# Kernel optimization log

Hardware: AMD Instinct MI355X
Metric: run time of the kernel (lower is better)

The kernel has to match this reference:

```python
import jax, jax.numpy as jnp
import numpy as np

MARGIN = 0.3
EPS = 1e-6  # torch.nn.functional.pairwise_distance eps


def setup_inputs() -> dict:
    key = jax.random.key(0)
    k1, k2 = jax.random.split(key)
    B, D, C = 8192, 256, 512
    embeddings = jax.random.normal(k1, (B, D), dtype=jnp.float32)
    labels = jax.random.randint(k2, (B,), 0, C, dtype=jnp.int64)
    return {"embeddings": embeddings, "labels": labels}


def reference(embeddings, labels):
    B = embeddings.shape[0]
    # pairwise squared L2 via GEMM
    dot = embeddings @ embeddings.T                      # [B, B]
    sq = jnp.diag(dot)[:, None] + jnp.diag(dot)[None, :] - 2.0 * dot
    dist_sq = jnp.clip(sq, 0.0)

    same = labels[:, None] == labels[None, :]            # [B, B] bool
    eye = jnp.eye(B, dtype=bool)
    pos_mask = same & ~eye
    neg_mask = ~same

    valid = pos_mask.any(axis=1) & neg_mask.any(axis=1)  # [B]
    INF = dist_sq.max() + 1.0

    hardest_pos_idx = jnp.argmax(dist_sq * pos_mask.astype(dist_sq.dtype), axis=1)
    hardest_neg_idx = jnp.argmin(dist_sq + same.astype(dist_sq.dtype) * INF, axis=1)

    a = embeddings
    p = embeddings[hardest_pos_idx]
    n = embeddings[hardest_neg_idx]
    # torch pairwise_distance: ||x1 - x2 + eps||_2
    d_ap = jnp.linalg.norm(a - p + EPS, axis=1)
    d_an = jnp.linalg.norm(a - n + EPS, axis=1)
    per_anchor = jnp.maximum(d_ap - d_an + MARGIN, 0.0)

    v = valid.astype(per_anchor.dtype)
    n_valid = v.sum()
    loss = jnp.where(n_valid > 0, (per_anchor * v).sum() / jnp.maximum(n_valid, 1.0), 0.0)
    return loss
```

## Files before the change

kernel.cpp:

```cpp
#include <hip/hip_runtime.h>
#include <math.h>

#define NB 8192
#define ND 256
#define MARGIN_F 0.3f
#define EPS_F 1e-6f
#define BIAS_F 512.0f
#define NFIN 2048

typedef __attribute__((ext_vector_type(8))) short bf16x8;
typedef __attribute__((ext_vector_type(4))) float f32x4;

__device__ __forceinline__ unsigned short f2bf(float x) {
    unsigned int u = __float_as_uint(x);
    return (unsigned short)((u + 0x7fffu + ((u >> 16) & 1u)) >> 16);
}

__device__ __forceinline__ void gld16(const void* g, void* l) {
    __builtin_amdgcn_global_load_lds(
        (const __attribute__((address_space(1))) void*)g,
        (__attribute__((address_space(3))) void*)l, 16, 0, 0);
}

__global__ __launch_bounds__(512) void prep_k(const float* __restrict__ emb,
                                              unsigned short* __restrict__ ehi,
                                              float* __restrict__ sqnb,
                                              unsigned int* __restrict__ pos_key,
                                              unsigned int* __restrict__ neg_key) {
    __shared__ float sm[8][16];
    const int tid = threadIdx.x;
    const int tk = tid >> 6;
    const int lane = tid & 63;
    const int q = lane >> 4;
    const int lx = lane & 15;
    const int row = blockIdx.x * 16 + lx;
    const int k = tk * 32 + q * 8;

    const float4 v0 = *reinterpret_cast<const float4*>(&emb[(size_t)row * ND + k]);
    const float4 v1 = *reinterpret_cast<const float4*>(&emb[(size_t)row * ND + k + 4]);
    ushort4 h0, h1;
    h0.x = f2bf(v0.x); h0.y = f2bf(v0.y); h0.z = f2bf(v0.z); h0.w = f2bf(v0.w);
    h1.x = f2bf(v1.x); h1.y = f2bf(v1.y); h1.z = f2bf(v1.z); h1.w = f2bf(v1.w);
    *reinterpret_cast<ushort4*>(&ehi[(size_t)blockIdx.x * 4096 + tid * 8])     = h0;
    *reinterpret_cast<ushort4*>(&ehi[(size_t)blockIdx.x * 4096 + tid * 8 + 4]) = h1;

    if (tid >= 32 && tid < 48) pos_key[blockIdx.x * 16 + (tid - 32)] = 0u;
    if (tid >= 48 && tid < 64) neg_key[blockIdx.x * 16 + (tid - 48)] = 0xFFFFFFFFu;

    float s = v0.x * v0.x + v0.y * v0.y + v0.z * v0.z + v0.w * v0.w
            + v1.x * v1.x + v1.y * v1.y + v1.z * v1.z + v1.w * v1.w;
    s += __shfl_xor(s, 16, 64);
    s += __shfl_xor(s, 32, 64);
    if (q == 0) sm[tk][lx] = s;
    __syncthreads();
    if (tid < 16) {
        float t = 0.0f;
#pragma unroll
        for (int wv = 0; wv < 8; ++wv) t += sm[wv][tid];
        sqnb[blockIdx.x * 16 + tid] = t + BIAS_F;
    }
}

template <bool DIAG>
__device__ __forceinline__ void mine_tile(
        const f32x4 (&acc)[2][4], const float (&sqjc)[4], const int (&lblc)[4],
        const unsigned (&enc)[4], const int* __restrict__ lbl_i_s,
        unsigned (&pmax)[8], unsigned (&nmin)[8],
        int i_base, int jb, int wrow, int q, int lx) {
#pragma unroll
    for (int tr = 0; tr < 2; ++tr) {
#pragma unroll
        for (int reg = 0; reg < 4; ++reg) {
            const int r = tr * 4 + reg;
            const int rowb = wrow + tr * 16 + q * 4 + reg;
            const int lab = lbl_i_s[rowb];
            unsigned pk[4], nk[4];
#pragma unroll
            for (int tc = 0; tc < 4; ++tc) {
                const float v = fmaf(-2.0f, acc[tr][tc][reg], sqjc[tc]);
                const unsigned key = (__float_as_uint(v) & 0xFFFFE000u) | enc[tc];
                const bool same = (lblc[tc] == lab);
                bool pc = same;
                if (DIAG) pc = same && ((jb + tc * 16 + lx) != (i_base + rowb));
                pk[tc] = pc ? key : 0u;
                nk[tc] = same ? 0xFFFFFFFFu : key;
            }
            const unsigned pa = pk[0] >= pk[1] ? pk[0] : pk[1];
            const unsigned pb = pk[2] >= pk[3] ? pk[2] : pk[3];
            const unsigned pm = pa >= pb ? pa : pb;
            pmax[r] = pmax[r] >= pm ? pmax[r] : pm;
            const unsigned na = nk[0] <= nk[1] ? nk[0] : nk[1];
            const unsigned nb = nk[2] <= nk[3] ? nk[2] : nk[3];
            const unsigned nm = na <= nb ? na : nb;
            nmin[r] = nmin[r] <= nm ? nmin[r] : nm;
        }
    }
}

__global__ __launch_bounds__(256, 4) void pair_k(
        const unsigned short* __restrict__ ehi, const float* __restrict__ sqnb,
        const int* __restrict__ labels,
        unsigned int* __restrict__ pos_key, unsigned int* __restrict__ neg_key) {
    __shared__ short Bsh[32 * 512];
    __shared__ int   lbl_i_s[128];

    const int tid = threadIdx.x;
    const int w = tid >> 6;
    const int lane = tid & 63;
    const int q = lane >> 4;
    const int lx = lane & 15;
    const int bid = blockIdx.x;
    const int slice = bid & 15;
    const int i_base = (bid >> 4) * 128;
    const int wrow = w * 32;
    const int g0 = (i_base >> 4) + w * 2;

    if (tid < 128) lbl_i_s[tid] = labels[i_base + tid];

    unsigned pmax[8], nmin[8];
#pragma unroll
    for (int r = 0; r < 8; ++r) { pmax[r] = 0u; nmin[r] = 0xFFFFFFFFu; }

#pragma unroll 1
    for (int jt = 0; jt < 8; ++jt) {
        const int jb = slice * 512 + jt * 64;
        __syncthreads();
        {
            const unsigned short* srcB = ehi + (size_t)(jb >> 4) * 4096;
#pragma unroll
            for (int p = 0; p < 8; ++p)
                gld16(srcB + ((size_t)p * 256 + tid) * 8, Bsh + (p * 256 + tid) * 8);
        }
        int lblc[4]; float sqjc[4]; unsigned enc[4];
#pragma unroll
        for (int tc = 0; tc < 4; ++tc) {
            const int jj = jb + tc * 16 + lx;
            lblc[tc] = labels[jj];
            sqjc[tc] = sqnb[jj];
            enc[tc] = 8191u - (unsigned)jj;
        }
        bf16x8 a0[2], a1[2];
#pragma unroll
        for (int tr = 0; tr < 2; ++tr)
            a0[tr] = *(const bf16x8*)&ehi[((size_t)(g0 + tr) * 8 + 0) * 512 + lane * 8];
        __syncthreads();

        f32x4 acc[2][4];
#pragma unroll
        for (int a = 0; a < 2; ++a)
#pragma unroll
            for (int b = 0; b < 4; ++b) acc[a][b] = (f32x4){0.f, 0.f, 0.f, 0.f};

#pragma unroll 1
        for (int kb2 = 0; kb2 < 4; ++kb2) {
            const int kbe = kb2 * 2, kbo = kbe + 1;
#pragma unroll
            for (int tr = 0; tr < 2; ++tr)
                a1[tr] = *(const bf16x8*)&ehi[((size_t)(g0 + tr) * 8 + kbo) * 512 + lane * 8];
            {
                bf16x8 bh[4];
#pragma unroll
                for (int tc = 0; tc < 4; ++tc)
                    bh[tc] = *(const bf16x8*)&Bsh[(tc * 8 + kbe) * 512 + lane * 8];
#pragma unroll
                for (int tr = 0; tr < 2; ++tr)
#pragma unroll
                    for (int tc = 0; tc < 4; ++tc)
                        acc[tr][tc] = __builtin_amdgcn_mfma_f32_16x16x32_bf16(
                            a0[tr], bh[tc], acc[tr][tc], 0, 0, 0);
            }
            const int kbn = (kbe + 2) & 7;
#pragma unroll
            for (int tr = 0; tr < 2; ++tr)
                a0[tr] = *(const bf16x8*)&ehi[((size_t)(g0 + tr) * 8 + kbn) * 512 + lane * 8];
            {
                bf16x8 bh[4];
#pragma unroll
                for (int tc = 0; tc < 4; ++tc)
                    bh[tc] = *(const bf16x8*)&Bsh[(tc * 8 + kbo) * 512 + lane * 8];
#pragma unroll
                for (int tr = 0; tr < 2; ++tr)
#pragma unroll
                    for (int tc = 0; tc < 4; ++tc)
                        acc[tr][tc] = __builtin_amdgcn_mfma_f32_16x16x32_bf16(
                            a1[tr], bh[tc], acc[tr][tc], 0, 0, 0);
            }
        }

        if ((unsigned)(jb - i_base) < 128u)
            mine_tile<true>(acc, sqjc, lblc, enc, lbl_i_s, pmax, nmin, i_base, jb, wrow, q, lx);
        else
            mine_tile<false>(acc, sqjc, lblc, enc, lbl_i_s, pmax, nmin, i_base, jb, wrow, q, lx);
    }

#pragma unroll
    for (int r = 0; r < 8; ++r) {
        unsigned pm = pmax[r], nm = nmin[r];
#pragma unroll
        for (int mm = 1; mm < 16; mm <<= 1) {
            const unsigned pm2 = __shfl_xor(pm, mm, 64);
            const unsigned nm2 = __shfl_xor(nm, mm, 64);
            pm = pm >= pm2 ? pm : pm2;
            nm = nm <= nm2 ? nm : nm2;
        }
        if (lx == r) {
            const int row = i_base + wrow + (r >> 2) * 16 + q * 4 + (r & 3);
            atomicMax(&pos_key[row], pm);
            atomicMin(&neg_key[row], nm);
        }
    }
}

__global__ __launch_bounds__(256) void final_k(
        const float* __restrict__ emb,
        const unsigned int* __restrict__ pos_key, const unsigned int* __restrict__ neg_key,
        float* __restrict__ pbsum, float* __restrict__ pbcnt) {
    __shared__ float ssum[4], scnt[4];
    const int w = threadIdx.x >> 6;
    const int lane = threadIdx.x & 63;
    const int i = blockIdx.x * 4 + w;

    const unsigned pk = pos_key[i], nk = neg_key[i];
    const int pi = 8191 - (int)(pk & 8191u);
    const int ni = 8191 - (int)(nk & 8191u);
    const bool valid = (pk != 0u) && (nk != 0xFFFFFFFFu);

    const float4 av  = *reinterpret_cast<const float4*>(&emb[(size_t)i  * ND + lane * 4]);
    const float4 pvv = *reinterpret_cast<const float4*>(&emb[(size_t)pi * ND + lane * 4]);
    const float4 nvv = *reinterpret_cast<const float4*>(&emb[(size_t)ni * ND + lane * 4]);
    float sap, san;
    {
        const float d0 = av.x - pvv.x + EPS_F, d1 = av.y - pvv.y + EPS_F;
        const float d2 = av.z - pvv.z + EPS_F, d3 = av.w - pvv.w + EPS_F;
        sap = d0 * d0 + d1 * d1 + d2 * d2 + d3 * d3;
        const float e0 = av.x - nvv.x + EPS_F, e1 = av.y - nvv.y + EPS_F;
        const float e2 = av.z - nvv.z + EPS_F, e3 = av.w - nvv.w + EPS_F;
        san = e0 * e0 + e1 * e1 + e2 * e2 + e3 * e3;
    }
#pragma unroll
    for (int m = 32; m; m >>= 1) {
        sap += __shfl_down(sap, m, 64);
        san += __shfl_down(san, m, 64);
    }
    if (lane == 0) {
        const float per = fmaxf(sqrtf(sap) - sqrtf(san) + MARGIN_F, 0.0f);
        ssum[w] = valid ? per : 0.0f;
        scnt[w] = valid ? 1.0f : 0.0f;
    }
    __syncthreads();
    if (threadIdx.x == 0) {
        pbsum[blockIdx.x] = ssum[0] + ssum[1] + ssum[2] + ssum[3];
        pbcnt[blockIdx.x] = scnt[0] + scnt[1] + scnt[2] + scnt[3];
    }
}

__global__ __launch_bounds__(256) void reduce_k(const float* __restrict__ pbsum,
                                                const float* __restrict__ pbcnt,
                                                float* __restrict__ out) {
    __shared__ float fs[4], fc[4];
    const int tid = threadIdx.x;
    float s = 0.0f, c = 0.0f;
#pragma unroll
    for (int r = 0; r < NFIN / 256; ++r) {
        s += pbsum[r * 256 + tid];
        c += pbcnt[r * 256 + tid];
    }
#pragma unroll
    for (int m = 32; m; m >>= 1) { s += __shfl_down(s, m, 64); c += __shfl_down(c, m, 64); }
    const int wv = tid >> 6, lane = tid & 63;
    if (lane == 0) { fs[wv] = s; fc[wv] = c; }
    __syncthreads();
    if (tid == 0) {
        const float S = fs[0] + fs[1] + fs[2] + fs[3];
        const float C = fc[0] + fc[1] + fc[2] + fc[3];
        out[0] = (C > 0.0f) ? (S / fmaxf(C, 1.0f)) : 0.0f;
    }
}

extern "C" void kernel_launch(void* const* d_in, const int* in_sizes, int n_in,
                              void* d_out, int out_size, void* d_ws, size_t ws_size,
                              hipStream_t stream) {
    const float* emb = (const float*)d_in[0];
    const int* labels = (const int*)d_in[1];
    float* out = (float*)d_out;

    char* ws = (char*)d_ws;
    unsigned short* ehi = (unsigned short*)ws;
    float* sqnb = (float*)(ws + (size_t)NB * ND * 2);
    unsigned int* pos_key = (unsigned int*)(sqnb + NB);
    unsigned int* neg_key = pos_key + NB;
    float* pbsum = (float*)(neg_key + NB);
    float* pbcnt = pbsum + NFIN;

    hipLaunchKernelGGL(prep_k, dim3(NB / 16), dim3(512), 0, stream,
                       emb, ehi, sqnb, pos_key, neg_key);
    hipLaunchKernelGGL(pair_k, dim3(1024), dim3(256), 0, stream,
                       ehi, sqnb, labels, pos_key, neg_key);
    hipLaunchKernelGGL(final_k, dim3(NFIN), dim3(256), 0, stream,
                       emb, pos_key, neg_key, pbsum, pbcnt);
    hipLaunchKernelGGL(reduce_k, dim3(1), dim3(256), 0, stream, pbsum, pbcnt, out);
}
```

Baseline: 114.3 us.

## Hold A tile in registers, widen column tile, double-buffer B in LDS

The pair kernel now loads the whole 32x256 A fragment into registers once, with -2 scaling folded in by flipping the bf16 sign bit (and adjusting the exponent). B tiles widen to 128 columns and are double-buffered in LDS by K halves, so loads overlap MFMA work. Accumulators start at the column norm, which removes the FMA in mining, and row labels are cached in registers. Occupancy drops from 4 to 2 blocks per CU to make room for the extra registers, and the bit trick assumes no bf16 exponent edge cases.

Result: no change. 114.3 us (+0.0%).

```diff
diff --git a/kernel.cpp b/kernel.cpp
--- a/kernel.cpp
+++ b/kernel.cpp
@@ -10,6 +10,7 @@
 
 typedef __attribute__((ext_vector_type(8))) short bf16x8;
 typedef __attribute__((ext_vector_type(4))) float f32x4;
+typedef __attribute__((ext_vector_type(4))) unsigned int u32x4;
 
 __device__ __forceinline__ unsigned short f2bf(float x) {
     unsigned int u = __float_as_uint(x);
@@ -63,8 +64,8 @@
 
 template <bool DIAG>
 __device__ __forceinline__ void mine_tile(
-        const f32x4 (&acc)[2][4], const float (&sqjc)[4], const int (&lblc)[4],
-        const unsigned (&enc)[4], const int* __restrict__ lbl_i_s,
+        const f32x4 (&acc)[2][8], const int (&lblc)[8], const unsigned (&enc)[8],
+        const int (&labr)[8],
         unsigned (&pmax)[8], unsigned (&nmin)[8],
         int i_base, int jb, int wrow, int q, int lx) {
 #pragma unroll
@@ -72,37 +73,45 @@
 #pragma unroll
         for (int reg = 0; reg < 4; ++reg) {
             const int r = tr * 4 + reg;
-            const int rowb = wrow + tr * 16 + q * 4 + reg;
-            const int lab = lbl_i_s[rowb];
-            unsigned pk[4], nk[4];
-#pragma unroll
-            for (int tc = 0; tc < 4; ++tc) {
-                const float v = fmaf(-2.0f, acc[tr][tc][reg], sqjc[tc]);
+            const int lab = labr[r];
+            const int rowg = i_base + wrow + tr * 16 + q * 4 + reg;
+            unsigned pk[8], nk[8];
+#pragma unroll
+            for (int tc = 0; tc < 8; ++tc) {
+                const float v = acc[tr][tc][reg];
                 const unsigned key = (__float_as_uint(v) & 0xFFFFE000u) | enc[tc];
                 const bool same = (lblc[tc] == lab);
                 bool pc = same;
-                if (DIAG) pc = same && ((jb + tc * 16 + lx) != (i_base + rowb));
+                if (DIAG) pc = same && ((jb + tc * 16 + lx) != rowg);
                 pk[tc] = pc ? key : 0u;
                 nk[tc] = same ? 0xFFFFFFFFu : key;
             }
             const unsigned pa = pk[0] >= pk[1] ? pk[0] : pk[1];
             const unsigned pb = pk[2] >= pk[3] ? pk[2] : pk[3];
-            const unsigned pm = pa >= pb ? pa : pb;
+            const unsigned pc2 = pk[4] >= pk[5] ? pk[4] : pk[5];
+            const unsigned pd = pk[6] >= pk[7] ? pk[6] : pk[7];
+            const unsigned pe = pa >= pb ? pa : pb;
+            const unsigned pf = pc2 >= pd ? pc2 : pd;
+            const unsigned pm = pe >= pf ? pe : pf;
             pmax[r] = pmax[r] >= pm ? pmax[r] : pm;
             const unsigned na = nk[0] <= nk[1] ? nk[0] : nk[1];
             const unsigned nb = nk[2] <= nk[3] ? nk[2] : nk[3];
-            const unsigned nm = na <= nb ? na : nb;
+            const unsigned nc = nk[4] <= nk[5] ? nk[4] : nk[5];
+            const unsigned nd = nk[6] <= nk[7] ? nk[6] : nk[7];
+            const unsigned ne = na <= nb ? na : nb;
+            const unsigned nf = nc <= nd ? nc : nd;
+            const unsigned nm = ne <= nf ? ne : nf;
             nmin[r] = nmin[r] <= nm ? nmin[r] : nm;
         }
     }
 }
 
-__global__ __launch_bounds__(256, 4) void pair_k(
+__global__ __launch_bounds__(256, 2) void pair_k(
         const unsigned short* __restrict__ ehi, const float* __restrict__ sqnb,
         const int* __restrict__ labels,
         unsigned int* __restrict__ pos_key, unsigned int* __restrict__ neg_key) {
-    __shared__ short Bsh[32 * 512];
-    __shared__ int   lbl_i_s[128];
+    __shared__ short Bsh[2][16384];
+    __shared__ __align__(16) int lbl_i_s[128];
 
     const int tid = threadIdx.x;
     const int w = tid >> 6;
@@ -113,84 +122,107 @@
     const int slice = bid & 15;
     const int i_base = (bid >> 4) * 128;
     const int wrow = w * 32;
-    const int g0 = (i_base >> 4) + w * 2;
+    const int ga0 = (i_base >> 4) + w * 2;
 
     if (tid < 128) lbl_i_s[tid] = labels[i_base + tid];
 
+    {
+        const unsigned short* src = ehi + (size_t)(slice * 32) * 4096;
+#pragma unroll
+        for (int p = 0; p < 8; ++p)
+            gld16(src + (size_t)p * 4096 + tid * 8, &Bsh[0][(p * 256 + tid) * 8]);
+    }
+
+    bf16x8 a[2][8];
+#pragma unroll
+    for (int tr = 0; tr < 2; ++tr)
+#pragma unroll
+        for (int s = 0; s < 8; ++s) {
+            union { u32x4 u; bf16x8 h; } cv;
+            cv.u = *reinterpret_cast<const u32x4*>(
+                &ehi[((size_t)(ga0 + tr) * 8 + s) * 512 + lane * 8]);
+            cv.u = (cv.u ^ 0x80008000u) + 0x00800080u;
+            a[tr][s] = cv.h;
+        }
+
     unsigned pmax[8], nmin[8];
 #pragma unroll
     for (int r = 0; r < 8; ++r) { pmax[r] = 0u; nmin[r] = 0xFFFFFFFFu; }
 
+    __syncthreads();
+
+    int labr[8];
+    {
+        const int4 l0 = *reinterpret_cast<const int4*>(&lbl_i_s[wrow + q * 4]);
+        const int4 l1 = *reinterpret_cast<const int4*>(&lbl_i_s[wrow + 16 + q * 4]);
+        labr[0] = l0.x; labr[1] = l0.y; labr[2] = l0.z; labr[3] = l0.w;
+        labr[4] = l1.x; labr[5] = l1.y; labr[6] = l1.z; labr[7] = l1.w;
+    }
+
 #pragma unroll 1
-    for (int jt = 0; jt < 8; ++jt) {
-        const int jb = slice * 512 + jt * 64;
-        __syncthreads();
-        {
-            const unsigned short* srcB = ehi + (size_t)(jb >> 4) * 4096;
-#pragma unroll
-            for (int p = 0; p < 8; ++p)
-                gld16(srcB + ((size_t)p * 256 + tid) * 8, Bsh + (p * 256 + tid) * 8);
-        }
-        int lblc[4]; float sqjc[4]; unsigned enc[4];
-#pragma unroll
-        for (int tc = 0; tc < 4; ++tc) {
+    for (int jt = 0; jt < 4; ++jt) {
+        const int jb = slice * 512 + jt * 128;
+
+        int lblc[8]; unsigned enc[8];
+        f32x4 acc[2][8];
+#pragma unroll
+        for (int tc = 0; tc < 8; ++tc) {
             const int jj = jb + tc * 16 + lx;
             lblc[tc] = labels[jj];
-            sqjc[tc] = sqnb[jj];
             enc[tc] = 8191u - (unsigned)jj;
-        }
-        bf16x8 a0[2], a1[2];
-#pragma unroll
-        for (int tr = 0; tr < 2; ++tr)
-            a0[tr] = *(const bf16x8*)&ehi[((size_t)(g0 + tr) * 8 + 0) * 512 + lane * 8];
+            const float sj = sqnb[jj];
+            acc[0][tc] = (f32x4){sj, sj, sj, sj};
+            acc[1][tc] = (f32x4){sj, sj, sj, sj};
+        }
+
+        {
+            const unsigned short* src = ehi + (size_t)(jb >> 4) * 4096 + 2048;
+#pragma unroll
+            for (int p = 0; p < 8; ++p)
+                gld16(src + (size_t)p * 4096 + tid * 8, &Bsh[1][(p * 256 + tid) * 8]);
+        }
+        __builtin_amdgcn_s_setprio(1);
+#pragma unroll
+        for (int kb = 0; kb < 4; ++kb) {
+#pragma unroll
+            for (int tc = 0; tc < 8; ++tc) {
+                const bf16x8 bh = *reinterpret_cast<const bf16x8*>(
+                    &Bsh[0][(tc * 4 + kb) * 512 + lane * 8]);
+                acc[0][tc] = __builtin_amdgcn_mfma_f32_16x16x32_bf16(
+                    a[0][kb], bh, acc[0][tc], 0, 0, 0);
+                acc[1][tc] = __builtin_amdgcn_mfma_f32_16x16x32_bf16(
+                    a[1][kb], bh, acc[1][tc], 0, 0, 0);
+            }
+        }
+        __builtin_amdgcn_s_setprio(0);
         __syncthreads();
 
-        f32x4 acc[2][4];
-#pragma unroll
-        for (int a = 0; a < 2; ++a)
-#pragma unroll
-            for (int b = 0; b < 4; ++b) acc[a][b] = (f32x4){0.f, 0.f, 0.f, 0.f};
-
-#pragma unroll 1
-        for (int kb2 = 0; kb2 < 4; ++kb2) {
-            const int kbe = kb2 * 2, kbo = kbe + 1;
-#pragma unroll
-            for (int tr = 0; tr < 2; ++tr)
-                a1[tr] = *(const bf16x8*)&ehi[((size_t)(g0 + tr) * 8 + kbo) * 512 + lane * 8];
-            {
-                bf16x8 bh[4];
-#pragma unroll
-                for (int tc = 0; tc < 4; ++tc)
-                    bh[tc] = *(const bf16x8*)&Bsh[(tc * 8 + kbe) * 512 + lane * 8];
-#pragma unroll
-                for (int tr = 0; tr < 2; ++tr)
-#pragma unroll
-                    for (int tc = 0; tc < 4; ++tc)
-                        acc[tr][tc] = __builtin_amdgcn_mfma_f32_16x16x32_bf16(
-                            a0[tr], bh[tc], acc[tr][tc], 0, 0, 0);
+        if (jt < 3) {
+            const unsigned short* src = ehi + (size_t)((jb + 128) >> 4) * 4096;
+#pragma unroll
+            for (int p = 0; p < 8; ++p)
+                gld16(src + (size_t)p * 4096 + tid * 8, &Bsh[0][(p * 256 + tid) * 8]);
+        }
+        __builtin_amdgcn_s_setprio(1);
+#pragma unroll
+        for (int kb = 0; kb < 4; ++kb) {
+#pragma unroll
+            for (int tc = 0; tc < 8; ++tc) {
+                const bf16x8 bh = *reinterpret_cast<const bf16x8*>(
+                    &Bsh[1][(tc * 4 + kb) * 512 + lane * 8]);
+                acc[0][tc] = __builtin_amdgcn_mfma_f32_16x16x32_bf16(
+                    a[0][4 + kb], bh, acc[0][tc], 0, 0, 0);
+                acc[1][tc] = __builtin_amdgcn_mfma_f32_16x16x32_bf16(
+                    a[1][4 + kb], bh, acc[1][tc], 0, 0, 0);
             }
-            const int kbn = (kbe + 2) & 7;
-#pragma unroll
-            for (int tr = 0; tr < 2; ++tr)
-                a0[tr] = *(const bf16x8*)&ehi[((size_t)(g0 + tr) * 8 + kbn) * 512 + lane * 8];
-            {
-                bf16x8 bh[4];
-#pragma unroll
-                for (int tc = 0; tc < 4; ++tc)
-                    bh[tc] = *(const bf16x8*)&Bsh[(tc * 8 + kbo) * 512 + lane * 8];
-#pragma unroll
-                for (int tr = 0; tr < 2; ++tr)
-#pragma unroll
-                    for (int tc = 0; tc < 4; ++tc)
-                        acc[tr][tc] = __builtin_amdgcn_mfma_f32_16x16x32_bf16(
-                            a1[tr], bh[tc], acc[tr][tc], 0, 0, 0);
-            }
-        }
-
-        if ((unsigned)(jb - i_base) < 128u)
-            mine_tile<true>(acc, sqjc, lblc, enc, lbl_i_s, pmax, nmin, i_base, jb, wrow, q, lx);
+        }
+        __builtin_amdgcn_s_setprio(0);
+        __syncthreads();
+
+        if (jb == i_base)
+            mine_tile<true>(acc, lblc, enc, labr, pmax, nmin, i_base, jb, wrow, q, lx);
         else
-            mine_tile<false>(acc, sqjc, lblc, enc, lbl_i_s, pmax, nmin, i_base, jb, wrow, q, lx);
+            mine_tile<false>(acc, lblc, enc, labr, pmax, nmin, i_base, jb, wrow, q, lx);
     }
 
 #pragma unroll
```

## Enlarge pair tiles, keep A in registers, double-buffer B, fold sq-norm into accumulator

Applied to the files above, without the earlier changes.

The pair kernel now gives each block 256 rows, and each wave 64 rows held entirely in registers with the sign flipped so the MFMA computes -dot. The B tiles are double-buffered in LDS in K halves, and the accumulator is initialised with the column squared norm, so mining reads the distance directly and compares floats with fmax/fmin. The separate reduce kernel is removed: final_k uses a last-block ticket to do the global reduction, saving one launch. The larger register footprint (64 bf16x8 A fragments plus 16 accumulators) may cut occupancy. The tiling also changes to 32 slices of 256 columns.

Result: slower. 251.7 us (+120.2%).

```diff
diff --git a/kernel.cpp b/kernel.cpp
--- a/kernel.cpp
+++ b/kernel.cpp
@@ -7,9 +7,11 @@
 #define EPS_F 1e-6f
 #define BIAS_F 512.0f
 #define NFIN 2048
+#define NEG_INIT 0x7F800000u
 
 typedef __attribute__((ext_vector_type(8))) short bf16x8;
 typedef __attribute__((ext_vector_type(4))) float f32x4;
+typedef __attribute__((ext_vector_type(4))) unsigned int u32x4;
 
 __device__ __forceinline__ unsigned short f2bf(float x) {
     unsigned int u = __float_as_uint(x);
@@ -26,7 +28,8 @@
                                               unsigned short* __restrict__ ehi,
                                               float* __restrict__ sqnb,
                                               unsigned int* __restrict__ pos_key,
-                                              unsigned int* __restrict__ neg_key) {
+                                              unsigned int* __restrict__ neg_key,
+                                              unsigned int* __restrict__ ticket) {
     __shared__ float sm[8][16];
     const int tid = threadIdx.x;
     const int tk = tid >> 6;
@@ -45,7 +48,8 @@
     *reinterpret_cast<ushort4*>(&ehi[(size_t)blockIdx.x * 4096 + tid * 8 + 4]) = h1;
 
     if (tid >= 32 && tid < 48) pos_key[blockIdx.x * 16 + (tid - 32)] = 0u;
-    if (tid >= 48 && tid < 64) neg_key[blockIdx.x * 16 + (tid - 48)] = 0xFFFFFFFFu;
+    if (tid >= 48 && tid < 64) neg_key[blockIdx.x * 16 + (tid - 48)] = NEG_INIT;
+    if (blockIdx.x == 0 && tid == 0) atomicExch(ticket, 0u);
 
     float s = v0.x * v0.x + v0.y * v0.y + v0.z * v0.z + v0.w * v0.w
             + v1.x * v1.x + v1.y * v1.y + v1.z * v1.z + v1.w * v1.w;
@@ -63,36 +67,32 @@
 
 template <bool DIAG>
 __device__ __forceinline__ void mine_tile(
-        const f32x4 (&acc)[2][4], const float (&sqjc)[4], const int (&lblc)[4],
-        const unsigned (&enc)[4], const int* __restrict__ lbl_i_s,
-        unsigned (&pmax)[8], unsigned (&nmin)[8],
-        int i_base, int jb, int wrow, int q, int lx) {
-#pragma unroll
-    for (int tr = 0; tr < 2; ++tr) {
+        const f32x4 (&acc)[4][4], const int (&lblc)[4], const unsigned (&enc)[4],
+        const int (&labr)[16], float (&pmax)[16], float (&nmin)[16],
+        int jb, int wr_base, int q, int lx) {
+    const float NEGF = __uint_as_float(NEG_INIT);
+#pragma unroll
+    for (int tr = 0; tr < 4; ++tr) {
 #pragma unroll
         for (int reg = 0; reg < 4; ++reg) {
             const int r = tr * 4 + reg;
-            const int rowb = wrow + tr * 16 + q * 4 + reg;
-            const int lab = lbl_i_s[rowb];
-            unsigned pk[4], nk[4];
+            const int lab = labr[r];
+            const int rowg = wr_base + tr * 16 + q * 4 + reg;
+            float pk[4], nk[4];
 #pragma unroll
             for (int tc = 0; tc < 4; ++tc) {
-                const float v = fmaf(-2.0f, acc[tr][tc][reg], sqjc[tc]);
-                const unsigned key = (__float_as_uint(v) & 0xFFFFE000u) | enc[tc];
+                const unsigned kb = (__float_as_uint(acc[tr][tc][reg]) & 0xFFFFE000u) | enc[tc];
+                const float keyf = __uint_as_float(kb);
                 const bool same = (lblc[tc] == lab);
                 bool pc = same;
-                if (DIAG) pc = same && ((jb + tc * 16 + lx) != (i_base + rowb));
-                pk[tc] = pc ? key : 0u;
-                nk[tc] = same ? 0xFFFFFFFFu : key;
+                if (DIAG) pc = same && ((jb + tc * 16 + lx) != rowg);
+                pk[tc] = pc ? keyf : 0.0f;
+                nk[tc] = same ? NEGF : keyf;
             }
-            const unsigned pa = pk[0] >= pk[1] ? pk[0] : pk[1];
-            const unsigned pb = pk[2] >= pk[3] ? pk[2] : pk[3];
-            const unsigned pm = pa >= pb ? pa : pb;
-            pmax[r] = pmax[r] >= pm ? pmax[r] : pm;
-            const unsigned na = nk[0] <= nk[1] ? nk[0] : nk[1];
-            const unsigned nb = nk[2] <= nk[3] ? nk[2] : nk[3];
-            const unsigned nm = na <= nb ? na : nb;
-            nmin[r] = nmin[r] <= nm ? nmin[r] : nm;
+            const float t0 = fmaxf(fmaxf(pk[0], pk[1]), pk[2]);
+            pmax[r] = fmaxf(fmaxf(t0, pk[3]), pmax[r]);
+            const float t1 = fminf(fminf(nk[0], nk[1]), nk[2]);
+            nmin[r] = fminf(fminf(t1, nk[3]), nmin[r]);
         }
     }
 }
@@ -101,8 +101,8 @@
         const unsigned short* __restrict__ ehi, const float* __restrict__ sqnb,
         const int* __restrict__ labels,
         unsigned int* __restrict__ pos_key, unsigned int* __restrict__ neg_key) {
-    __shared__ short Bsh[32 * 512];
-    __shared__ int   lbl_i_s[128];
+    __shared__ short Bsh[2][8192];
+    __shared__ __align__(16) int lbl_i_s[256];
 
     const int tid = threadIdx.x;
     const int w = tid >> 6;
@@ -110,103 +110,115 @@
     const int q = lane >> 4;
     const int lx = lane & 15;
     const int bid = blockIdx.x;
-    const int slice = bid & 15;
-    const int i_base = (bid >> 4) * 128;
-    const int wrow = w * 32;
-    const int g0 = (i_base >> 4) + w * 2;
-
-    if (tid < 128) lbl_i_s[tid] = labels[i_base + tid];
-
-    unsigned pmax[8], nmin[8];
-#pragma unroll
-    for (int r = 0; r < 8; ++r) { pmax[r] = 0u; nmin[r] = 0xFFFFFFFFu; }
+    const int slice = bid & 31;
+    const int i_base = (bid >> 5) * 256;
+    const int wrow = w * 64;
+    const int wr_base = i_base + wrow;
+    const int ga0 = wr_base >> 4;
+
+    lbl_i_s[tid] = labels[i_base + tid];
+
+#define STAGE(JT, KH, BUF)                                                      \
+    do {                                                                        \
+        const unsigned short* _src =                                            \
+            ehi + ((size_t)((slice * 16 + (JT) * 4) * 8 + (KH) * 4)) * 512;     \
+        _Pragma("unroll")                                                       \
+        for (int p = 0; p < 4; ++p)                                             \
+            gld16(_src + ((size_t)(p * 8 + w)) * 512 + lane * 8,                \
+                  &Bsh[BUF][(p * 4 + w) * 512 + lane * 8]);                     \
+    } while (0)
+
+    STAGE(0, 0, 0);
+
+    bf16x8 a[4][8];
+#pragma unroll
+    for (int tr = 0; tr < 4; ++tr)
+#pragma unroll
+        for (int s = 0; s < 8; ++s) {
+            union { u32x4 u; bf16x8 h; } cv;
+            cv.u = *reinterpret_cast<const u32x4*>(
+                &ehi[((size_t)(ga0 + tr) * 8 + s) * 512 + lane * 8]);
+            cv.u = (cv.u ^ 0x80008000u) + 0x00800080u;
+            a[tr][s] = cv.h;
+        }
+
+    float pmax[16], nmin[16];
+    const float NEGF = __uint_as_float(NEG_INIT);
+#pragma unroll
+    for (int r = 0; r < 16; ++r) { pmax[r] = 0.0f; nmin[r] = NEGF; }
+
+    __syncthreads();
+
+    int labr[16];
+#pragma unroll
+    for (int tr = 0; tr < 4; ++tr) {
+        const int4 l = *reinterpret_cast<const int4*>(&lbl_i_s[wrow + tr * 16 + q * 4]);
+        labr[tr * 4 + 0] = l.x; labr[tr * 4 + 1] = l.y;
+        labr[tr * 4 + 2] = l.z; labr[tr * 4 + 3] = l.w;
+    }
+
+#define PHASE(BUF, S0)                                                          \
+    do {                                                                        \
+        __builtin_amdgcn_s_setprio(1);                                          \
+        _Pragma("unroll")                                                       \
+        for (int kb = 0; kb < 4; ++kb) {                                        \
+            _Pragma("unroll")                                                   \
+            for (int tc = 0; tc < 4; ++tc) {                                    \
+                const bf16x8 bh = *reinterpret_cast<const bf16x8*>(             \
+                    &Bsh[BUF][(tc * 4 + kb) * 512 + lane * 8]);                 \
+                _Pragma("unroll")                                               \
+                for (int tr = 0; tr < 4; ++tr)                                  \
+                    acc[tr][tc] = __builtin_amdgcn_mfma_f32_16x16x32_bf16(      \
+                        a[tr][(S0) + kb], bh, acc[tr][tc], 0, 0, 0);            \
+            }                                                                   \
+        }                                                                       \
+        __builtin_amdgcn_s_setprio(0);                                          \
+    } while (0)
 
 #pragma unroll 1
-    for (int jt = 0; jt < 8; ++jt) {
-        const int jb = slice * 512 + jt * 64;
-        __syncthreads();
-        {
-            const unsigned short* srcB = ehi + (size_t)(jb >> 4) * 4096;
-#pragma unroll
-            for (int p = 0; p < 8; ++p)
-                gld16(srcB + ((size_t)p * 256 + tid) * 8, Bsh + (p * 256 + tid) * 8);
-        }
-        int lblc[4]; float sqjc[4]; unsigned enc[4];
+    for (int jt = 0; jt < 4; ++jt) {
+        const int jb = slice * 256 + jt * 64;
+
+        STAGE(jt, 1, 1);
+
+        int lblc[4]; unsigned enc[4];
+        f32x4 acc[4][4];
 #pragma unroll
         for (int tc = 0; tc < 4; ++tc) {
             const int jj = jb + tc * 16 + lx;
             lblc[tc] = labels[jj];
-            sqjc[tc] = sqnb[jj];
             enc[tc] = 8191u - (unsigned)jj;
-        }
-        bf16x8 a0[2], a1[2];
-#pragma unroll
-        for (int tr = 0; tr < 2; ++tr)
-            a0[tr] = *(const bf16x8*)&ehi[((size_t)(g0 + tr) * 8 + 0) * 512 + lane * 8];
+            const float sj = sqnb[jj];
+#pragma unroll
+            for (int tr = 0; tr < 4; ++tr) acc[tr][tc] = (f32x4){sj, sj, sj, sj};
+        }
+
+        PHASE(0, 0);
         __syncthreads();
-
-        f32x4 acc[2][4];
-#pragma unroll
-        for (int a = 0; a < 2; ++a)
-#pragma unroll
-            for (int b = 0; b < 4; ++b) acc[a][b] = (f32x4){0.f, 0.f, 0.f, 0.f};
-
-#pragma unroll 1
-        for (int kb2 = 0; kb2 < 4; ++kb2) {
-            const int kbe = kb2 * 2, kbo = kbe + 1;
-#pragma unroll
-            for (int tr = 0; tr < 2; ++tr)
-                a1[tr] = *(const bf16x8*)&ehi[((size_t)(g0 + tr) * 8 + kbo) * 512 + lane * 8];
-            {
-                bf16x8 bh[4];
-#pragma unroll
-                for (int tc = 0; tc < 4; ++tc)
-                    bh[tc] = *(const bf16x8*)&Bsh[(tc * 8 + kbe) * 512 + lane * 8];
-#pragma unroll
-                for (int tr = 0; tr < 2; ++tr)
-#pragma unroll
-                    for (int tc = 0; tc < 4; ++tc)
-                        acc[tr][tc] = __builtin_amdgcn_mfma_f32_16x16x32_bf16(
-                            a0[tr], bh[tc], acc[tr][tc], 0, 0, 0);
-            }
-            const int kbn = (kbe + 2) & 7;
-#pragma unroll
-            for (int tr = 0; tr < 2; ++tr)
-                a0[tr] = *(const bf16x8*)&ehi[((size_t)(g0 + tr) * 8 + kbn) * 512 + lane * 8];
-            {
-                bf16x8 bh[4];
-#pragma unroll
-                for (int tc = 0; tc < 4; ++tc)
-                    bh[tc] = *(const bf16x8*)&Bsh[(tc * 8 + kbo) * 512 + lane * 8];
-#pragma unroll
-                for (int tr = 0; tr < 2; ++tr)
-#pragma unroll
-                    for (int tc = 0; tc < 4; ++tc)
-                        acc[tr][tc] = __builtin_amdgcn_mfma_f32_16x16x32_bf16(
-                            a1[tr], bh[tc], acc[tr][tc], 0, 0, 0);
-            }
-        }
-
-        if ((unsigned)(jb - i_base) < 128u)
-            mine_tile<true>(acc, sqjc, lblc, enc, lbl_i_s, pmax, nmin, i_base, jb, wrow, q, lx);
+        if (jt < 3) STAGE(jt + 1, 0, 0);
+        PHASE(1, 4);
+        __syncthreads();
+
+        if (jb == wr_base)
+            mine_tile<true>(acc, lblc, enc, labr, pmax, nmin, jb, wr_base, q, lx);
         else
-            mine_tile<false>(acc, sqjc, lblc, enc, lbl_i_s, pmax, nmin, i_base, jb, wrow, q, lx);
-    }
-
-#pragma unroll
-    for (int r = 0; r < 8; ++r) {
-        unsigned pm = pmax[r], nm = nmin[r];
+            mine_tile<false>(acc, lblc, enc, labr, pmax, nmin, jb, wr_base, q, lx);
+    }
+#undef STAGE
+#undef PHASE
+
+#pragma unroll
+    for (int r = 0; r < 16; ++r) {
+        float pm = pmax[r], nm = nmin[r];
 #pragma unroll
         for (int mm = 1; mm < 16; mm <<= 1) {
-            const unsigned pm2 = __shfl_xor(pm, mm, 64);
-            const unsigned nm2 = __shfl_xor(nm, mm, 64);
-            pm = pm >= pm2 ? pm : pm2;
-            nm = nm <= nm2 ? nm : nm2;
+            pm = fmaxf(pm, __shfl_xor(pm, mm, 64));
+            nm = fminf(nm, __shfl_xor(nm, mm, 64));
         }
         if (lx == r) {
-            const int row = i_base + wrow + (r >> 2) * 16 + q * 4 + (r & 3);
-            atomicMax(&pos_key[row], pm);
-            atomicMin(&neg_key[row], nm);
+            const int row = wr_base + (r >> 2) * 16 + q * 4 + (r & 3);
+            atomicMax(&pos_key[row], __float_as_uint(pm));
+            atomicMin(&neg_key[row], __float_as_uint(nm));
         }
     }
 }
@@ -214,16 +226,19 @@
 __global__ __launch_bounds__(256) void final_k(
         const float* __restrict__ emb,
         const unsigned int* __restrict__ pos_key, const unsigned int* __restrict__ neg_key,
-        float* __restrict__ pbsum, float* __restrict__ pbcnt) {
+        float* __restrict__ pbsum, float* __restrict__ pbcnt,
+        unsigned int* __restrict__ ticket, float* __restrict__ out) {
     __shared__ float ssum[4], scnt[4];
-    const int w = threadIdx.x >> 6;
-    const int lane = threadIdx.x & 63;
+    __shared__ unsigned int last;
+    const int tid = threadIdx.x;
+    const int w = tid >> 6;
+    const int lane = tid & 63;
     const int i = blockIdx.x * 4 + w;
 
     const unsigned pk = pos_key[i], nk = neg_key[i];
     const int pi = 8191 - (int)(pk & 8191u);
     const int ni = 8191 - (int)(nk & 8191u);
-    const bool valid = (pk != 0u) && (nk != 0xFFFFFFFFu);
+    const bool valid = (pk != 0u) && (nk != NEG_INIT);
 
     const float4 av  = *reinterpret_cast<const float4*>(&emb[(size_t)i  * ND + lane * 4]);
     const float4 pvv = *reinterpret_cast<const float4*>(&emb[(size_t)pi * ND + lane * 4]);
@@ -248,32 +263,30 @@
         scnt[w] = valid ? 1.0f : 0.0f;
     }
     __syncthreads();
-    if (threadIdx.x == 0) {
+    if (tid == 0) {
         pbsum[blockIdx.x] = ssum[0] + ssum[1] + ssum[2] + ssum[3];
         pbcnt[blockIdx.x] = scnt[0] + scnt[1] + scnt[2] + scnt[3];
-    }
-}
-
-__global__ __launch_bounds__(256) void reduce_k(const float* __restrict__ pbsum,
-                                                const float* __restrict__ pbcnt,
-                                                float* __restrict__ out) {
-    __shared__ float fs[4], fc[4];
-    const int tid = threadIdx.x;
-    float s = 0.0f, c = 0.0f;
-#pragma unroll
-    for (int r = 0; r < NFIN / 256; ++r) {
-        s += pbsum[r * 256 + tid];
-        c += pbcnt[r * 256 + tid];
-    }
-#pragma unroll
-    for (int m = 32; m; m >>= 1) { s += __shfl_down(s, m, 64); c += __shfl_down(c, m, 64); }
-    const int wv = tid >> 6, lane = tid & 63;
-    if (lane == 0) { fs[wv] = s; fc[wv] = c; }
+        __threadfence();
+        last = (atomicAdd(ticket, 1u) == (unsigned)(NFIN - 1)) ? 1u : 0u;
+    }
     __syncthreads();
-    if (tid == 0) {
-        const float S = fs[0] + fs[1] + fs[2] + fs[3];
-        const float C = fc[0] + fc[1] + fc[2] + fc[3];
-        out[0] = (C > 0.0f) ? (S / fmaxf(C, 1.0f)) : 0.0f;
+    if (last != 0u) {
+        __shared__ float fs[4], fc[4];
+        float s = 0.0f, c = 0.0f;
+#pragma unroll
+        for (int r = 0; r < NFIN / 256; ++r) {
+            s += atomicAdd(&pbsum[r * 256 + tid], 0.0f);
+            c += atomicAdd(&pbcnt[r * 256 + tid], 0.0f);
+        }
+#pragma unroll
+        for (int m = 32; m; m >>= 1) { s += __shfl_down(s, m, 64); c += __shfl_down(c, m, 64); }
+        if (lane == 0) { fs[w] = s; fc[w] = c; }
+        __syncthreads();
+        if (tid == 0) {
+            const float S = fs[0] + fs[1] + fs[2] + fs[3];
+            const float C = fc[0] + fc[1] + fc[2] + fc[3];
+            out[0] = (C > 0.0f) ? (S / fmaxf(C, 1.0f)) : 0.0f;
+        }
     }
 }
 
@@ -291,12 +304,12 @@
     unsigned int* neg_key = pos_key + NB;
     float* pbsum = (float*)(neg_key + NB);
     float* pbcnt = pbsum + NFIN;
+    unsigned int* ticket = (unsigned int*)(pbcnt + NFIN);
 
     hipLaunchKernelGGL(prep_k, dim3(NB / 16), dim3(512), 0, stream,
-                       emb, ehi, sqnb, pos_key, neg_key);
+                       emb, ehi, sqnb, pos_key, neg_key, ticket);
     hipLaunchKernelGGL(pair_k, dim3(1024), dim3(256), 0, stream,
                        ehi, sqnb, labels, pos_key, neg_key);
     hipLaunchKernelGGL(final_k, dim3(NFIN), dim3(256), 0, stream,
-                       emb, pos_key, neg_key, pbsum, pbcnt);
-    hipLaunchKernelGGL(reduce_k, dim3(1), dim3(256), 0, stream, pbsum, pbcnt, out);
-}
+                       emb, pos_key, neg_key, pbsum, pbcnt, ticket, out);
+}
```

## Double-buffer B tiles by K-half and fold column norms into MFMA accumulator init

Applied to the files above, without the earlier changes.

The B tile in LDS is split into two K-halves held in separate buffers. The next half's global-to-LDS load is issued while MFMAs run on the current half, and all A fragments for a half are preloaded, with setprio raised around the MFMA blocks. The -2·dot+sq_j epilogue is removed by starting the accumulator at -0.5·sq_j. Mining then works on float min/max keys, and negative-biased floats are reinterpreted so the existing unsigned atomics still order correctly. This adds register pressure from the preloaded A fragments. Correctness depends on the bias keeping every accumulator value negative so that float and uint orderings stay consistent.

Measured after the change: 116.5 us. About the same (+1.9%).

```diff
diff --git a/kernel.cpp b/kernel.cpp
--- a/kernel.cpp
+++ b/kernel.cpp
@@ -63,10 +63,12 @@
 
 template <bool DIAG>
 __device__ __forceinline__ void mine_tile(
-        const f32x4 (&acc)[2][4], const float (&sqjc)[4], const int (&lblc)[4],
-        const unsigned (&enc)[4], const int* __restrict__ lbl_i_s,
-        unsigned (&pmax)[8], unsigned (&nmin)[8],
+        const f32x4 (&acc)[2][4], const int (&lblc)[4], const unsigned (&enc)[4],
+        const int* __restrict__ lbl_i_s,
+        float (&pkey)[8], float (&nkey)[8],
         int i_base, int jb, int wrow, int q, int lx) {
+    const float PINF = __uint_as_float(0x7F800000u);
+    const float NINF = __uint_as_float(0xFF800000u);
 #pragma unroll
     for (int tr = 0; tr < 2; ++tr) {
 #pragma unroll
@@ -74,25 +76,21 @@
             const int r = tr * 4 + reg;
             const int rowb = wrow + tr * 16 + q * 4 + reg;
             const int lab = lbl_i_s[rowb];
-            unsigned pk[4], nk[4];
+            float pk[4], nk[4];
 #pragma unroll
             for (int tc = 0; tc < 4; ++tc) {
-                const float v = fmaf(-2.0f, acc[tr][tc][reg], sqjc[tc]);
-                const unsigned key = (__float_as_uint(v) & 0xFFFFE000u) | enc[tc];
+                const float keyf = __uint_as_float(
+                    (__float_as_uint(acc[tr][tc][reg]) & 0xFFFFE000u) | enc[tc]);
                 const bool same = (lblc[tc] == lab);
                 bool pc = same;
                 if (DIAG) pc = same && ((jb + tc * 16 + lx) != (i_base + rowb));
-                pk[tc] = pc ? key : 0u;
-                nk[tc] = same ? 0xFFFFFFFFu : key;
+                pk[tc] = pc ? keyf : PINF;
+                nk[tc] = same ? NINF : keyf;
             }
-            const unsigned pa = pk[0] >= pk[1] ? pk[0] : pk[1];
-            const unsigned pb = pk[2] >= pk[3] ? pk[2] : pk[3];
-            const unsigned pm = pa >= pb ? pa : pb;
-            pmax[r] = pmax[r] >= pm ? pmax[r] : pm;
-            const unsigned na = nk[0] <= nk[1] ? nk[0] : nk[1];
-            const unsigned nb = nk[2] <= nk[3] ? nk[2] : nk[3];
-            const unsigned nm = na <= nb ? na : nb;
-            nmin[r] = nmin[r] <= nm ? nmin[r] : nm;
+            const float t0 = fminf(fminf(pk[0], pk[1]), pk[2]);
+            pkey[r] = fminf(fminf(t0, pk[3]), pkey[r]);
+            const float t1 = fmaxf(fmaxf(nk[0], nk[1]), nk[2]);
+            nkey[r] = fmaxf(fmaxf(t1, nk[3]), nkey[r]);
         }
     }
 }
@@ -101,8 +99,8 @@
         const unsigned short* __restrict__ ehi, const float* __restrict__ sqnb,
         const int* __restrict__ labels,
         unsigned int* __restrict__ pos_key, unsigned int* __restrict__ neg_key) {
-    __shared__ short Bsh[32 * 512];
-    __shared__ int   lbl_i_s[128];
+    __shared__ __align__(16) short Bsh[2][8192];
+    __shared__ int lbl_i_s[128];
 
     const int tid = threadIdx.x;
     const int w = tid >> 6;
@@ -117,21 +115,40 @@
 
     if (tid < 128) lbl_i_s[tid] = labels[i_base + tid];
 
-    unsigned pmax[8], nmin[8];
-#pragma unroll
-    for (int r = 0; r < 8; ++r) { pmax[r] = 0u; nmin[r] = 0xFFFFFFFFu; }
+#define STAGE(JT, KH, BUF)                                                            \
+    do {                                                                              \
+        _Pragma("unroll")                                                             \
+        for (int p = 0; p < 4; ++p)                                                   \
+            gld16(ehi + (size_t)((slice * 32 + (JT) * 4 + p) * 8 + (KH) * 4) * 512    \
+                      + tid * 8,                                                      \
+                  &Bsh[BUF][(p * 256 + tid) * 8]);                                    \
+    } while (0)
+
+#define AFRAG(TR, KB)                                                                 \
+    (*reinterpret_cast<const bf16x8*>(                                                \
+        &ehi[((size_t)(g0 + (TR)) * 8 + (KB)) * 512 + lane * 8]))
+
+    STAGE(0, 0, 0);
+
+    float pkey[8], nkey[8];
+    const float PINF = __uint_as_float(0x7F800000u);
+    const float NINF = __uint_as_float(0xFF800000u);
+#pragma unroll
+    for (int r = 0; r < 8; ++r) { pkey[r] = PINF; nkey[r] = NINF; }
+
+    __syncthreads();
 
 #pragma unroll 1
     for (int jt = 0; jt < 8; ++jt) {
         const int jb = slice * 512 + jt * 64;
-        __syncthreads();
-        {
-            const unsigned short* srcB = ehi + (size_t)(jb >> 4) * 4096;
-#pragma unroll
-            for (int p = 0; p < 8; ++p)
-                gld16(srcB + ((size_t)p * 256 + tid) * 8, Bsh + (p * 256 + tid) * 8);
-        }
-        int lblc[4]; float sqjc[4]; unsigned enc[4];
+
+        bf16x8 aA[4][2];
+#pragma unroll
+        for (int kb = 0; kb < 4; ++kb)
+#pragma unroll
+            for (int tr = 0; tr < 2; ++tr) aA[kb][tr] = AFRAG(tr, kb);
+
+        int lblc[4]; unsigned enc[4]; float sqjc[4];
 #pragma unroll
         for (int tc = 0; tc < 4; ++tc) {
             const int jj = jb + tc * 16 + lx;
@@ -139,74 +156,80 @@
             sqjc[tc] = sqnb[jj];
             enc[tc] = 8191u - (unsigned)jj;
         }
-        bf16x8 a0[2], a1[2];
-#pragma unroll
-        for (int tr = 0; tr < 2; ++tr)
-            a0[tr] = *(const bf16x8*)&ehi[((size_t)(g0 + tr) * 8 + 0) * 512 + lane * 8];
+
+        STAGE(jt, 1, 1);
+
+        f32x4 acc[2][4];
+#pragma unroll
+        for (int tc = 0; tc < 4; ++tc) {
+            const float s0 = -0.5f * sqjc[tc];
+#pragma unroll
+            for (int tr = 0; tr < 2; ++tr) acc[tr][tc] = (f32x4){s0, s0, s0, s0};
+        }
+
+        __builtin_amdgcn_s_setprio(1);
+#pragma unroll
+        for (int kb = 0; kb < 4; ++kb) {
+#pragma unroll
+            for (int tc = 0; tc < 4; ++tc) {
+                const bf16x8 bh = *reinterpret_cast<const bf16x8*>(
+                    &Bsh[0][(tc * 4 + kb) * 512 + lane * 8]);
+#pragma unroll
+                for (int tr = 0; tr < 2; ++tr)
+                    acc[tr][tc] = __builtin_amdgcn_mfma_f32_16x16x32_bf16(
+                        aA[kb][tr], bh, acc[tr][tc], 0, 0, 0);
+            }
+        }
+        __builtin_amdgcn_s_setprio(0);
         __syncthreads();
 
-        f32x4 acc[2][4];
-#pragma unroll
-        for (int a = 0; a < 2; ++a)
-#pragma unroll
-            for (int b = 0; b < 4; ++b) acc[a][b] = (f32x4){0.f, 0.f, 0.f, 0.f};
-
-#pragma unroll 1
-        for (int kb2 = 0; kb2 < 4; ++kb2) {
-            const int kbe = kb2 * 2, kbo = kbe + 1;
-#pragma unroll
-            for (int tr = 0; tr < 2; ++tr)
-                a1[tr] = *(const bf16x8*)&ehi[((size_t)(g0 + tr) * 8 + kbo) * 512 + lane * 8];
-            {
-                bf16x8 bh[4];
-#pragma unroll
-                for (int tc = 0; tc < 4; ++tc)
-                    bh[tc] = *(const bf16x8*)&Bsh[(tc * 8 + kbe) * 512 + lane * 8];
+        bf16x8 aB[4][2];
+#pragma unroll
+        for (int kb = 0; kb < 4; ++kb)
+#pragma unroll
+            for (int tr = 0; tr < 2; ++tr) aB[kb][tr] = AFRAG(tr, kb + 4);
+
+        if (jt < 7) STAGE(jt + 1, 0, 0);
+
+        __builtin_amdgcn_s_setprio(1);
+#pragma unroll
+        for (int kb = 0; kb < 4; ++kb) {
+#pragma unroll
+            for (int tc = 0; tc < 4; ++tc) {
+                const bf16x8 bh = *reinterpret_cast<const bf16x8*>(
+                    &Bsh[1][(tc * 4 + kb) * 512 + lane * 8]);
 #pragma unroll
                 for (int tr = 0; tr < 2; ++tr)
-#pragma unroll
-                    for (int tc = 0; tc < 4; ++tc)
-                        acc[tr][tc] = __builtin_amdgcn_mfma_f32_16x16x32_bf16(
-                            a0[tr], bh[tc], acc[tr][tc], 0, 0, 0);
+                    acc[tr][tc] = __builtin_amdgcn_mfma_f32_16x16x32_bf16(
+                        aB[kb][tr], bh, acc[tr][tc], 0, 0, 0);
             }
-            const int kbn = (kbe + 2) & 7;
-#pragma unroll
-            for (int tr = 0; tr < 2; ++tr)
-                a0[tr] = *(const bf16x8*)&ehi[((size_t)(g0 + tr) * 8 + kbn) * 512 + lane * 8];
-            {
-                bf16x8 bh[4];
-#pragma unroll
-                for (int tc = 0; tc < 4; ++tc)
-                    bh[tc] = *(const bf16x8*)&Bsh[(tc * 8 + kbo) * 512 + lane * 8];
-#pragma unroll
-                for (int tr = 0; tr < 2; ++tr)
-#pragma unroll
-                    for (int tc = 0; tc < 4; ++tc)
-                        acc[tr][tc] = __builtin_amdgcn_mfma_f32_16x16x32_bf16(
-                            a1[tr], bh[tc], acc[tr][tc], 0, 0, 0);
-            }
-        }
+        }
+        __builtin_amdgcn_s_setprio(0);
 
         if ((unsigned)(jb - i_base) < 128u)
-            mine_tile<true>(acc, sqjc, lblc, enc, lbl_i_s, pmax, nmin, i_base, jb, wrow, q, lx);
+            mine_tile<true>(acc, lblc, enc, lbl_i_s, pkey, nkey, i_base, jb, wrow, q, lx);
         else
-            mine_tile<false>(acc, sqjc, lblc, enc, lbl_i_s, pmax, nmin, i_base, jb, wrow, q, lx);
-    }
+            mine_tile<false>(acc, lblc, enc, lbl_i_s, pkey, nkey, i_base, jb, wrow, q, lx);
+
+        __syncthreads();
+    }
+#undef STAGE
+#undef AFRAG
 
 #pragma unroll
     for (int r = 0; r < 8; ++r) {
-        unsigned pm = pmax[r], nm = nmin[r];
+        float pm = pkey[r], nm = nkey[r];
 #pragma unroll
         for (int mm = 1; mm < 16; mm <<= 1) {
-            const unsigned pm2 = __shfl_xor(pm, mm, 64);
-            const unsigned nm2 = __shfl_xor(nm, mm, 64);
-            pm = pm >= pm2 ? pm : pm2;
-            nm = nm <= nm2 ? nm : nm2;
+            pm = fminf(pm, __shfl_xor(pm, mm, 64));
+            nm = fmaxf(nm, __shfl_xor(nm, mm, 64));
         }
         if (lx == r) {
             const int row = i_base + wrow + (r >> 2) * 16 + q * 4 + (r & 3);
-            atomicMax(&pos_key[row], pm);
-            atomicMin(&neg_key[row], nm);
+            const unsigned pmb = (pm == PINF) ? 0u : __float_as_uint(pm);
+            const unsigned nmb = (nm == NINF) ? 0xFFFFFFFFu : __float_as_uint(nm);
+            atomicMax(&pos_key[row], pmb);
+            atomicMin(&neg_key[row], nmb);
         }
     }
 }
```
